# Performance work log

Measured on AMD Instinct MI355X. Metric: run time of the kernel, lower is better.

## Reference

```python
import jax, jax.numpy as jnp
import numpy as np

B, T, D, H = 2, 2048, 1024, 16
HD = D // H  # 64


def setup_inputs() -> dict:
    key = jax.random.key(0)
    ks = jax.random.split(key, 9)
    s = 1.0 / np.sqrt(D)
    return {
        "x": jax.random.normal(ks[0], (B, T, D), dtype=jnp.float32),
        "Wq": jax.random.uniform(ks[1], (D, D), minval=-s, maxval=s, dtype=jnp.float32),
        "bq": jax.random.uniform(ks[2], (D,), minval=-s, maxval=s, dtype=jnp.float32),
        "Wk": jax.random.uniform(ks[3], (D, D), minval=-s, maxval=s, dtype=jnp.float32),
        "bk": jax.random.uniform(ks[4], (D,), minval=-s, maxval=s, dtype=jnp.float32),
        "Wv": jax.random.uniform(ks[5], (D, D), minval=-s, maxval=s, dtype=jnp.float32),
        "bv": jax.random.uniform(ks[6], (D,), minval=-s, maxval=s, dtype=jnp.float32),
        "Wo": jax.random.uniform(ks[7], (D, D), minval=-s, maxval=s, dtype=jnp.float32),
        "bo": jax.random.uniform(ks[8], (D,), minval=-s, maxval=s, dtype=jnp.float32),
    }


def reference(x, Wq, bq, Wk, bk, Wv, bv, Wo, bo):
    b, t, d = x.shape
    # projections (nn.Linear: x @ W.T + b), split heads -> [B,H,T,hd]
    def split_heads(y):
        return y.reshape(b, t, H, HD).transpose(0, 2, 1, 3)
    Q = split_heads(x @ Wq.T + bq)
    K = split_heads(x @ Wk.T + bk)
    V = split_heads(x @ Wv.T + bv)
    # causal linear attention via cumulative outer-product state
    # Z[b,h,s,p,n] = V[b,h,s,p] * K[b,h,s,n]
    Z = jnp.einsum('bhsp,bhsn->bhspn', V, K)
    Z_cum = jnp.cumsum(Z, axis=2)  # prefix sum over time -> causal state
    Y = jnp.einsum('bhtn,bhtpn->bhtp', Q, Z_cum)  # [B,H,T,hd]
    Y = Y.transpose(0, 2, 1, 3).reshape(b, t, d)
    return Y @ Wo.T + bo
```

## Files before the change

kernel.cpp:

```cpp
#include <hip/hip_runtime.h>
#include <stdint.h>

#define B_  2
#define T_  2048
#define D_  1024
#define H_  16
#define HD_ 64
#define M_  (B_*T_)
#define CHK 128
#define NC  (T_/CHK)
#define BH  (B_*H_)

#define XN   4194304
#define WN   1048576

typedef unsigned short ushort_t;
typedef unsigned int   uint_t;

typedef __bf16 bf16x8 __attribute__((ext_vector_type(8)));
typedef float  f32x4  __attribute__((ext_vector_type(4)));

__device__ inline ushort_t f2bf(float f) {
    uint_t x = __float_as_uint(f);
    x += 0x7fffu + ((x >> 16) & 1u);
    return (ushort_t)(x >> 16);
}

__device__ inline uint4 pack8(const float4& lo, const float4& hi) {
    uint4 pk;
    pk.x = (uint_t)f2bf(lo.x) | ((uint_t)f2bf(lo.y) << 16);
    pk.y = (uint_t)f2bf(lo.z) | ((uint_t)f2bf(lo.w) << 16);
    pk.z = (uint_t)f2bf(hi.x) | ((uint_t)f2bf(hi.y) << 16);
    pk.w = (uint_t)f2bf(hi.z) | ((uint_t)f2bf(hi.w) << 16);
    return pk;
}

__global__ __launch_bounds__(256) void to_bf16_all(
    const float* __restrict__ x,  const float* __restrict__ Wq,
    const float* __restrict__ Wk, const float* __restrict__ Wv,
    const float* __restrict__ Wo, ushort_t* __restrict__ dst)
{
    const int idx = blockIdx.x * 256 + threadIdx.x;
    const int e   = idx * 8;
    const float* src;
    if      (e < XN)          src = x  + e;
    else if (e < XN + WN)     src = Wq + (e - XN);
    else if (e < XN + 2*WN)   src = Wk + (e - XN - WN);
    else if (e < XN + 3*WN)   src = Wv + (e - XN - 2*WN);
    else                      src = Wo + (e - XN - 3*WN);
    float4 lo = ((const float4*)src)[0];
    float4 hi = ((const float4*)src)[1];
    *(uint4*)(dst + e) = pack8(lo, hi);
}

__device__ inline void stage_rows(const ushort_t* __restrict__ g, ushort_t* ldsw,
                                  int lane, int issues) {
    const int rr  = lane >> 3;
    const int kg8 = ((lane & 7) ^ rr) << 3;
    const ushort_t* src = g + (size_t)rr * D_ + kg8;
    #pragma unroll
    for (int i = 0; i < issues; i++) {
        __builtin_amdgcn_global_load_lds(
            (const __attribute__((address_space(1))) void*)(src + (size_t)(i * 8) * D_),
            (__attribute__((address_space(3))) void*)(ldsw + i * 512),
            16, 0, 0);
    }
}

__global__ __launch_bounds__(256) void gemm_qkv(
    const ushort_t* __restrict__ xb, const ushort_t* __restrict__ Wqkvb,
    const float* __restrict__ bq, const float* __restrict__ bk,
    const float* __restrict__ bv, ushort_t* __restrict__ qkv_ws)
{
    const int flat = blockIdx.x;
    const int r    = flat & 7;
    const int j    = flat >> 3;
    const int mt   = ((r >> 1) << 4) | (j & 15);
    const int nt   = ((r & 1) << 2) | ((j >> 4) & 3);
    const int z    = j >> 6;

    const ushort_t* W  = Wqkvb + (size_t)z * WN;
    const float*    bi = (z == 0) ? bq : ((z == 1) ? bk : bv);
    ushort_t* out = qkv_ws + (size_t)z * (size_t)M_ * D_;

    __shared__ __align__(16) ushort_t As[64 * 64];
    __shared__ __align__(16) ushort_t Bs[128 * 64];

    const int tid  = threadIdx.x;
    const int m0   = mt * 64;
    const int n0   = nt * 128;
    const int wave = tid >> 6;
    const int lane = tid & 63;
    const int wm   = (wave >> 1) * 32;
    const int wn   = (wave & 1) * 64;
    const int fr   = lane & 15;
    const int quad = lane >> 4;

    const ushort_t* Ag = xb + (size_t)(m0 + wave * 16) * D_;
    const ushort_t* Bg = W  + (size_t)(n0 + wave * 32) * D_;
    ushort_t* Alds = &As[wave * 16 * 64];
    ushort_t* Blds = &Bs[wave * 32 * 64];

    f32x4 acc[2][4];
    #pragma unroll
    for (int i = 0; i < 2; i++)
        #pragma unroll
        for (int j2 = 0; j2 < 4; j2++)
            acc[i][j2] = (f32x4){0.f, 0.f, 0.f, 0.f};

    for (int k0 = 0; k0 < D_; k0 += 64) {
        __syncthreads();
        stage_rows(Ag + k0, Alds, lane, 2);
        stage_rows(Bg + k0, Blds, lane, 4);
        __syncthreads();

        #pragma unroll
        for (int ksg = 0; ksg <= 4; ksg += 4) {
            const int kgo = ((ksg + quad) ^ (fr & 7)) << 3;
            bf16x8 af[2], bf[4];
            #pragma unroll
            for (int i = 0; i < 2; i++) {
                uint4 u = *(const uint4*)&As[(wm + i * 16 + fr) * 64 + kgo];
                af[i] = __builtin_bit_cast(bf16x8, u);
            }
            #pragma unroll
            for (int j2 = 0; j2 < 4; j2++) {
                uint4 u = *(const uint4*)&Bs[(wn + j2 * 16 + fr) * 64 + kgo];
                bf[j2] = __builtin_bit_cast(bf16x8, u);
            }
            #pragma unroll
            for (int i = 0; i < 2; i++)
                #pragma unroll
                for (int j2 = 0; j2 < 4; j2++)
                    acc[i][j2] = __builtin_amdgcn_mfma_f32_16x16x32_bf16(
                        af[i], bf[j2], acc[i][j2], 0, 0, 0);
        }
    }

    const int rb = quad * 4;
    #pragma unroll
    for (int j2 = 0; j2 < 4; j2++) {
        const int n = n0 + wn + j2 * 16 + fr;
        const float bias = bi[n];
        const int h  = n >> 6;
        const int hd = n & 63;
        #pragma unroll
        for (int i = 0; i < 2; i++) {
            #pragma unroll
            for (int rr = 0; rr < 4; rr++) {
                const int m = m0 + wm + i * 16 + rb + rr;
                const int b = m >> 11, t = m & (T_ - 1);
                out[(((size_t)(b * H_ + h)) * T_ + t) * HD_ + hd] =
                    f2bf(acc[i][j2][rr] + bias);
            }
        }
    }
}

__global__ __launch_bounds__(256) void gemm_out(
    const ushort_t* __restrict__ Yw, const ushort_t* __restrict__ Wob,
    const float* __restrict__ bo, float* __restrict__ out)
{
    const int flat = blockIdx.x;
    const int r    = flat & 7;
    const int j    = flat >> 3;
    const int mt   = ((r >> 1) << 4) | (j & 15);
    const int nt   = ((r & 1) << 2) | (j >> 4);

    __shared__ __align__(16) ushort_t As[64 * 64];
    __shared__ __align__(16) ushort_t Bs[128 * 64];

    const int tid  = threadIdx.x;
    const int m0   = mt * 64;
    const int n0   = nt * 128;
    const int wave = tid >> 6;
    const int lane = tid & 63;
    const int wm   = (wave >> 1) * 32;
    const int wn   = (wave & 1) * 64;
    const int fr   = lane & 15;
    const int quad = lane >> 4;

    const ushort_t* Ag = Yw  + (size_t)(m0 + wave * 16) * D_;
    const ushort_t* Bg = Wob + (size_t)(n0 + wave * 32) * D_;
    ushort_t* Alds = &As[wave * 16 * 64];
    ushort_t* Blds = &Bs[wave * 32 * 64];

    f32x4 acc[2][4];
    #pragma unroll
    for (int i = 0; i < 2; i++)
        #pragma unroll
        for (int j2 = 0; j2 < 4; j2++)
            acc[i][j2] = (f32x4){0.f, 0.f, 0.f, 0.f};

    for (int k0 = 0; k0 < D_; k0 += 64) {
        __syncthreads();
        stage_rows(Ag + k0, Alds, lane, 2);
        stage_rows(Bg + k0, Blds, lane, 4);
        __syncthreads();

        #pragma unroll
        for (int ksg = 0; ksg <= 4; ksg += 4) {
            const int kgo = ((ksg + quad) ^ (fr & 7)) << 3;
            bf16x8 af[2], bf[4];
            #pragma unroll
            for (int i = 0; i < 2; i++) {
                uint4 u = *(const uint4*)&As[(wm + i * 16 + fr) * 64 + kgo];
                af[i] = __builtin_bit_cast(bf16x8, u);
            }
            #pragma unroll
            for (int j2 = 0; j2 < 4; j2++) {
                uint4 u = *(const uint4*)&Bs[(wn + j2 * 16 + fr) * 64 + kgo];
                bf[j2] = __builtin_bit_cast(bf16x8, u);
            }
            #pragma unroll
            for (int i = 0; i < 2; i++)
                #pragma unroll
                for (int j2 = 0; j2 < 4; j2++)
                    acc[i][j2] = __builtin_amdgcn_mfma_f32_16x16x32_bf16(
                        af[i], bf[j2], acc[i][j2], 0, 0, 0);
        }
    }

    const int rb = quad * 4;
    #pragma unroll
    for (int j2 = 0; j2 < 4; j2++) {
        const int n = n0 + wn + j2 * 16 + fr;
        const float bias = bo[n];
        #pragma unroll
        for (int i = 0; i < 2; i++) {
            #pragma unroll
            for (int rr = 0; rr < 4; rr++) {
                const int m = m0 + wm + i * 16 + rb + rr;
                out[(size_t)m * D_ + n] = acc[i][j2][rr] + bias;
            }
        }
    }
}

#define LDS_ 136

__device__ inline void scatter_T(const uint4* u, ushort_t* dst, int tid) {
    #pragma unroll
    for (int g = 0; g < 4; g++) {
        const int v  = tid + 256 * g;
        const int s  = v >> 3;
        const int p8 = (v & 7) * 8;
        ushort_t e[8];
        *(uint4*)e = u[g];
        const int sb = s >> 3, slo = s & 7;
        #pragma unroll
        for (int j = 0; j < 8; j++) {
            const int p   = p8 + j;
            const int blk = (sb & 8) | ((sb ^ (p >> 3)) & 7);
            dst[p * LDS_ + (blk << 3) + slo] = e[j];
        }
    }
}

__device__ inline void stage_T(const ushort_t* __restrict__ src, ushort_t* dst, int tid) {
    uint4 u[4];
    #pragma unroll
    for (int g = 0; g < 4; g++) u[g] = ((const uint4*)src)[tid + 256 * g];
    scatter_T(u, dst, tid);
}

__device__ inline void stage_T512(const ushort_t* __restrict__ src, ushort_t* dst, int tid) {
    uint4 u[2];
    #pragma unroll
    for (int g = 0; g < 2; g++) u[g] = ((const uint4*)src)[tid + 512 * g];
    #pragma unroll
    for (int g = 0; g < 2; g++) {
        const int v  = tid + 512 * g;
        const int s  = v >> 3;
        const int p8 = (v & 7) * 8;
        ushort_t e[8];
        *(uint4*)e = u[g];
        const int sb = s >> 3, slo = s & 7;
        #pragma unroll
        for (int j = 0; j < 8; j++) {
            const int p   = p8 + j;
            const int blk = (sb & 8) | ((sb ^ (p >> 3)) & 7);
            dst[p * LDS_ + (blk << 3) + slo] = e[j];
        }
    }
}

__global__ __launch_bounds__(256) void chunk_delta(
    const ushort_t* __restrict__ k_ws, const ushort_t* __restrict__ v_ws,
    float* __restrict__ delta)
{
    const int c  = blockIdx.x;
    const int bh = blockIdx.y;
    __shared__ __align__(16) ushort_t VtS[64 * LDS_];
    __shared__ __align__(16) ushort_t KtS[64 * LDS_];

    const int tid  = threadIdx.x;
    const int wave = tid >> 6, lane = tid & 63;
    const int fr = lane & 15, quad = lane >> 4, rb = quad * 4;
    const int p  = wave * 16 + fr;

    const size_t base = ((size_t)bh * T_ + (size_t)c * CHK) * HD_;
    stage_T(v_ws + base, VtS, tid);
    stage_T(k_ws + base, KtS, tid);
    __syncthreads();

    f32x4 acc[4];
    #pragma unroll
    for (int jn = 0; jn < 4; jn++) acc[jn] = (f32x4){0.f, 0.f, 0.f, 0.f};

    #pragma unroll
    for (int kt = 0; kt < 4; kt++) {
        const int sb   = kt * 4 + quad;
        const int blkA = (sb & 8) | ((sb ^ (p >> 3)) & 7);
        bf16x8 af = __builtin_bit_cast(bf16x8,
            *(const uint4*)&VtS[p * LDS_ + (blkA << 3)]);
        #pragma unroll
        for (int jn = 0; jn < 4; jn++) {
            const int nr   = jn * 16 + fr;
            const int blkB = (sb & 8) | ((sb ^ (nr >> 3)) & 7);
            uint4 ub = *(const uint4*)&KtS[nr * LDS_ + (blkB << 3)];
            acc[jn] = __builtin_amdgcn_mfma_f32_16x16x32_bf16(
                af, __builtin_bit_cast(bf16x8, ub), acc[jn], 0, 0, 0);
        }
    }

    float* dp = delta + ((size_t)bh * NC + c) * 4096;
    #pragma unroll
    for (int jn = 0; jn < 4; jn++)
        #pragma unroll
        for (int r = 0; r < 4; r++)
            dp[(wave * 16 + rb + r) * 64 + jn * 16 + fr] = acc[jn][r];
}

__global__ __launch_bounds__(256) void states_prefix(
    const float* __restrict__ delta, ushort_t* __restrict__ states_bf)
{
    const int qd = blockIdx.x;
    const int bh = blockIdx.y;
    const size_t b0 = (size_t)bh * NC * 4096 + qd * 1024 + threadIdx.x;

    float s[4] = {0.f, 0.f, 0.f, 0.f};
    #pragma unroll
    for (int c = 0; c < NC; c++) {
        #pragma unroll
        for (int u = 0; u < 4; u++) {
            const size_t o = b0 + (size_t)c * 4096 + u * 256;
            states_bf[o] = f2bf(s[u]);
            s[u] += delta[o];
        }
    }
}

__global__ __launch_bounds__(512) void attn_chunk(
    const ushort_t* __restrict__ q_ws, const ushort_t* __restrict__ k_ws,
    const ushort_t* __restrict__ v_ws, const ushort_t* __restrict__ states_bf,
    ushort_t* __restrict__ y_ws)
{
    const int c = blockIdx.x, bh = blockIdx.y;
    __shared__ __align__(16) ushort_t VtS[64 * LDS_];
    __shared__ __align__(16) ushort_t Smat[128 * LDS_];

    const int tid  = threadIdx.x;
    const int wave = tid >> 6;
    const int lane = tid & 63;
    const int fr   = lane & 15;
    const int quad = lane >> 4;
    const int fk   = quad * 8;
    const int rb   = quad * 4;

    const size_t base = ((size_t)bh * T_ + (size_t)c * CHK) * HD_;
    const ushort_t* qg = q_ws + base;
    const ushort_t* kg = k_ws + base;
    const ushort_t* vg = v_ws + base;
    const ushort_t* st = states_bf + ((size_t)bh * NC + c) * 4096;

    stage_T512(vg, VtS, tid);
    __syncthreads();

    const int m = wave;

    bf16x8 aq[2];
    #pragma unroll
    for (int kk = 0; kk < 2; kk++) {
        uint4 u = *(const uint4*)(qg + (m * 16 + fr) * HD_ + kk * 32 + fk);
        aq[kk] = __builtin_bit_cast(bf16x8, u);
    }

    f32x4 acc[4];
    #pragma unroll
    for (int jn = 0; jn < 4; jn++) acc[jn] = (f32x4){0.f, 0.f, 0.f, 0.f};

    #pragma unroll
    for (int jn = 0; jn < 4; jn++) {
        #pragma unroll
        for (int kk = 0; kk < 2; kk++) {
            uint4 u = *(const uint4*)(st + (jn * 16 + fr) * 64 + kk * 32 + fk);
            bf16x8 bsp = __builtin_bit_cast(bf16x8, u);
            acc[jn] = __builtin_amdgcn_mfma_f32_16x16x32_bf16(
                aq[kk], bsp, acc[jn], 0, 0, 0);
        }
    }

    const int nk = (m + 2) >> 1;
    const int jt = 2 * nk;

    f32x4 sc[8];
    #pragma unroll
    for (int j = 0; j < 8; j++) sc[j] = (f32x4){0.f, 0.f, 0.f, 0.f};

    #pragma unroll
    for (int j = 0; j < 8; j++) {
        if (j <= m) {
            #pragma unroll
            for (int kk = 0; kk < 2; kk++) {
                uint4 u = *(const uint4*)(kg + (j * 16 + fr) * HD_ + kk * 32 + fk);
                sc[j] = __builtin_amdgcn_mfma_f32_16x16x32_bf16(
                    aq[kk], __builtin_bit_cast(bf16x8, u), sc[j], 0, 0, 0);
            }
        }
    }

    #pragma unroll
    for (int j = 0; j < 8; j++) {
        if (j < jt) {
            f32x4 v = sc[j];
            if (j == m) {
                #pragma unroll
                for (int r = 0; r < 4; r++)
                    if (fr > rb + r) v[r] = 0.f;
            }
            #pragma unroll
            for (int r = 0; r < 4; r++)
                Smat[(m * 16 + rb + r) * LDS_ + j * 16 + fr] = f2bf(v[r]);
        }
    }

    #pragma unroll
    for (int kt = 0; kt < 4; kt++) {
        if (kt < nk) {
            uint4 ua = *(const uint4*)&Smat[(m * 16 + fr) * LDS_ + kt * 32 + fk];
            bf16x8 as_ = __builtin_bit_cast(bf16x8, ua);
            #pragma unroll
            for (int jn = 0; jn < 4; jn++) {
                const int p   = jn * 16 + fr;
                const int sb  = kt * 4 + quad;
                const int blk = (sb & 8) | ((sb ^ (p >> 3)) & 7);
                uint4 ub = *(const uint4*)&VtS[p * LDS_ + (blk << 3)];
                acc[jn] = __builtin_amdgcn_mfma_f32_16x16x32_bf16(
                    as_, __builtin_bit_cast(bf16x8, ub), acc[jn], 0, 0, 0);
            }
        }
    }

    const int b = bh >> 4, h = bh & 15;
    ushort_t* yg = y_ws + ((size_t)(b * T_ + c * CHK)) * D_ + h * 64;
    #pragma unroll
    for (int jn = 0; jn < 4; jn++) {
        #pragma unroll
        for (int r = 0; r < 4; r++) {
            const int t = m * 16 + rb + r;
            const int p = jn * 16 + fr;
            yg[(size_t)t * D_ + p] = f2bf(acc[jn][r]);
        }
    }
}

extern "C" void kernel_launch(void* const* d_in, const int* in_sizes, int n_in,
                              void* d_out, int out_size, void* d_ws, size_t ws_size,
                              hipStream_t stream)
{
    const float* x  = (const float*)d_in[0];
    const float* Wq = (const float*)d_in[1];
    const float* bq = (const float*)d_in[2];
    const float* Wk = (const float*)d_in[3];
    const float* bk = (const float*)d_in[4];
    const float* Wv = (const float*)d_in[5];
    const float* bv = (const float*)d_in[6];
    const float* Wo = (const float*)d_in[7];
    const float* bo = (const float*)d_in[8];
    float* out = (float*)d_out;

    ushort_t* cvt    = (ushort_t*)d_ws;
    ushort_t* xb     = cvt;
    ushort_t* Wqkvb  = cvt + (size_t)XN;
    ushort_t* Wob    = cvt + (size_t)XN + 3 * WN;
    ushort_t* q_ws   = cvt + (size_t)XN + 4 * WN;
    ushort_t* k_ws   = q_ws + (size_t)M_ * D_;
    ushort_t* v_ws   = k_ws + (size_t)M_ * D_;
    ushort_t* y_ws   = v_ws + (size_t)M_ * D_;
    ushort_t* states_bf = Wqkvb;
    float*    delta  = (float*)(y_ws + (size_t)M_ * D_);

    to_bf16_all<<<dim3((XN + 4 * WN) / 8 / 256), 256, 0, stream>>>(
        x, Wq, Wk, Wv, Wo, cvt);
    gemm_qkv<<<dim3(1536), 256, 0, stream>>>(
        xb, Wqkvb, bq, bk, bv, q_ws);
    chunk_delta<<<dim3(NC, BH), 256, 0, stream>>>(k_ws, v_ws, delta);
    states_prefix<<<dim3(4, BH), 256, 0, stream>>>(delta, states_bf);
    attn_chunk<<<dim3(NC, BH), 512, 0, stream>>>(q_ws, k_ws, v_ws, states_bf, y_ws);
    gemm_out<<<dim3(512), 256, 0, stream>>>(y_ws, Wob, bo, out);
}
```

Baseline: 162.4 us.

## Fuse chunk-state prefix sum into attention kernel, drop states_prefix launch

Removes the separate states_prefix kernel, which ran a sequential scan over chunks using only 128 blocks. Each attn_chunk block now sums the fp32 deltas of all preceding chunks itself, converts the result to bf16 in shared memory, and feeds it to the MFMA inter-chunk term. Chunk 0 skips this term. This saves a launch and the low-parallelism scan, at the cost of redundant O(c) delta reads per block, up to 15 chunks of 16KB each.

```diff
diff --git a/kernel.cpp b/kernel.cpp
--- a/kernel.cpp
+++ b/kernel.cpp
@@ -332,33 +332,16 @@
             dp[(wave * 16 + rb + r) * 64 + jn * 16 + fr] = acc[jn][r];
 }
 
-__global__ __launch_bounds__(256) void states_prefix(
-    const float* __restrict__ delta, ushort_t* __restrict__ states_bf)
-{
-    const int qd = blockIdx.x;
-    const int bh = blockIdx.y;
-    const size_t b0 = (size_t)bh * NC * 4096 + qd * 1024 + threadIdx.x;
-
-    float s[4] = {0.f, 0.f, 0.f, 0.f};
-    #pragma unroll
-    for (int c = 0; c < NC; c++) {
-        #pragma unroll
-        for (int u = 0; u < 4; u++) {
-            const size_t o = b0 + (size_t)c * 4096 + u * 256;
-            states_bf[o] = f2bf(s[u]);
-            s[u] += delta[o];
-        }
-    }
-}
-
+#define STS_ 72
 __global__ __launch_bounds__(512) void attn_chunk(
     const ushort_t* __restrict__ q_ws, const ushort_t* __restrict__ k_ws,
-    const ushort_t* __restrict__ v_ws, const ushort_t* __restrict__ states_bf,
+    const ushort_t* __restrict__ v_ws, const float* __restrict__ delta,
     ushort_t* __restrict__ y_ws)
 {
     const int c = blockIdx.x, bh = blockIdx.y;
     __shared__ __align__(16) ushort_t VtS[64 * LDS_];
     __shared__ __align__(16) ushort_t Smat[128 * LDS_];
+    __shared__ __align__(16) ushort_t StS[64 * STS_];
 
     const int tid  = threadIdx.x;
     const int wave = tid >> 6;
@@ -372,9 +355,26 @@
     const ushort_t* qg = q_ws + base;
     const ushort_t* kg = k_ws + base;
     const ushort_t* vg = v_ws + base;
-    const ushort_t* st = states_bf + ((size_t)bh * NC + c) * 4096;
 
     stage_T512(vg, VtS, tid);
+
+    if (c > 0) {
+        float s[8];
+        #pragma unroll
+        for (int i = 0; i < 8; i++) s[i] = 0.f;
+        const float* dbase = delta + (size_t)bh * NC * 4096 + tid * 8;
+        for (int cc = 0; cc < c; cc++) {
+            const float* dp = dbase + (size_t)cc * 4096;
+            float4 a = ((const float4*)dp)[0];
+            float4 b = ((const float4*)dp)[1];
+            s[0] += a.x; s[1] += a.y; s[2] += a.z; s[3] += a.w;
+            s[4] += b.x; s[5] += b.y; s[6] += b.z; s[7] += b.w;
+        }
+        ushort_t ev[8];
+        #pragma unroll
+        for (int i = 0; i < 8; i++) ev[i] = f2bf(s[i]);
+        *(uint4*)&StS[(tid >> 3) * STS_ + (tid & 7) * 8] = *(uint4*)ev;
+    }
     __syncthreads();
 
     const int m = wave;
@@ -390,14 +390,16 @@
     #pragma unroll
     for (int jn = 0; jn < 4; jn++) acc[jn] = (f32x4){0.f, 0.f, 0.f, 0.f};
 
-    #pragma unroll
-    for (int jn = 0; jn < 4; jn++) {
-        #pragma unroll
-        for (int kk = 0; kk < 2; kk++) {
-            uint4 u = *(const uint4*)(st + (jn * 16 + fr) * 64 + kk * 32 + fk);
-            bf16x8 bsp = __builtin_bit_cast(bf16x8, u);
-            acc[jn] = __builtin_amdgcn_mfma_f32_16x16x32_bf16(
-                aq[kk], bsp, acc[jn], 0, 0, 0);
+    if (c > 0) {
+        #pragma unroll
+        for (int jn = 0; jn < 4; jn++) {
+            #pragma unroll
+            for (int kk = 0; kk < 2; kk++) {
+                uint4 u = *(const uint4*)&StS[(jn * 16 + fr) * STS_ + kk * 32 + fk];
+                bf16x8 bsp = __builtin_bit_cast(bf16x8, u);
+                acc[jn] = __builtin_amdgcn_mfma_f32_16x16x32_bf16(
+                    aq[kk], bsp, acc[jn], 0, 0, 0);
+            }
         }
     }
 
@@ -488,7 +490,6 @@
     ushort_t* k_ws   = q_ws + (size_t)M_ * D_;
     ushort_t* v_ws   = k_ws + (size_t)M_ * D_;
     ushort_t* y_ws   = v_ws + (size_t)M_ * D_;
-    ushort_t* states_bf = Wqkvb;
     float*    delta  = (float*)(y_ws + (size_t)M_ * D_);
 
     to_bf16_all<<<dim3((XN + 4 * WN) / 8 / 256), 256, 0, stream>>>(
@@ -496,7 +497,6 @@
     gemm_qkv<<<dim3(1536), 256, 0, stream>>>(
         xb, Wqkvb, bq, bk, bv, q_ws);
     chunk_delta<<<dim3(NC, BH), 256, 0, stream>>>(k_ws, v_ws, delta);
-    states_prefix<<<dim3(4, BH), 256, 0, stream>>>(delta, states_bf);
-    attn_chunk<<<dim3(NC, BH), 512, 0, stream>>>(q_ws, k_ws, v_ws, states_bf, y_ws);
+    attn_chunk<<<dim3(NC, BH), 512, 0, stream>>>(q_ws, k_ws, v_ws, delta, y_ws);
     gemm_out<<<dim3(512), 256, 0, stream>>>(y_ws, Wob, bo, out);
 }
```

Result: slower. 167.4 us (+3.1%).

## Fuse Q/K/V projections into one block sharing the staged x tile

Applied to the files above, without the earlier changes.

The QKV GEMM now has each 512-thread block compute a 128x64 tile for all three projections at once. The x tile is staged into LDS once and reused against three weight tiles, so x is read from memory a third as often. The grid shrinks from 1536 to 512 blocks. Each wave now holds 12 accumulators instead of 8, which raises register pressure, and the smaller grid may balance less evenly across CUs.

```diff
diff --git a/kernel.cpp b/kernel.cpp
--- a/kernel.cpp
+++ b/kernel.cpp
@@ -67,91 +67,100 @@
     }
 }
 
-__global__ __launch_bounds__(256) void gemm_qkv(
+__global__ __launch_bounds__(512) void gemm_qkv(
     const ushort_t* __restrict__ xb, const ushort_t* __restrict__ Wqkvb,
     const float* __restrict__ bq, const float* __restrict__ bk,
     const float* __restrict__ bv, ushort_t* __restrict__ qkv_ws)
 {
-    const int flat = blockIdx.x;
-    const int r    = flat & 7;
-    const int j    = flat >> 3;
-    const int mt   = ((r >> 1) << 4) | (j & 15);
-    const int nt   = ((r & 1) << 2) | ((j >> 4) & 3);
-    const int z    = j >> 6;
-
-    const ushort_t* W  = Wqkvb + (size_t)z * WN;
-    const float*    bi = (z == 0) ? bq : ((z == 1) ? bk : bv);
-    ushort_t* out = qkv_ws + (size_t)z * (size_t)M_ * D_;
-
-    __shared__ __align__(16) ushort_t As[64 * 64];
-    __shared__ __align__(16) ushort_t Bs[128 * 64];
+    const int bid = blockIdx.x;
+    const int r   = bid & 7;
+    const int j   = bid >> 3;
+    const int mt  = ((r >> 1) << 3) | (j & 7);
+    const int nt  = ((r & 1) << 3) | (j >> 3);
+    const int m0  = mt * 128;
+    const int n0  = nt * 64;
+
+    __shared__ __align__(16) ushort_t As[128 * 64];
+    __shared__ __align__(16) ushort_t Bs[3 * 64 * 64];
 
     const int tid  = threadIdx.x;
-    const int m0   = mt * 64;
-    const int n0   = nt * 128;
     const int wave = tid >> 6;
     const int lane = tid & 63;
     const int wm   = (wave >> 1) * 32;
-    const int wn   = (wave & 1) * 64;
+    const int wn   = (wave & 1) * 32;
     const int fr   = lane & 15;
     const int quad = lane >> 4;
+    const int rb   = quad * 4;
 
     const ushort_t* Ag = xb + (size_t)(m0 + wave * 16) * D_;
-    const ushort_t* Bg = W  + (size_t)(n0 + wave * 32) * D_;
     ushort_t* Alds = &As[wave * 16 * 64];
-    ushort_t* Blds = &Bs[wave * 32 * 64];
-
-    f32x4 acc[2][4];
-    #pragma unroll
-    for (int i = 0; i < 2; i++)
-        #pragma unroll
-        for (int j2 = 0; j2 < 4; j2++)
-            acc[i][j2] = (f32x4){0.f, 0.f, 0.f, 0.f};
+
+    f32x4 acc[3][2][2];
+    #pragma unroll
+    for (int z = 0; z < 3; z++)
+        #pragma unroll
+        for (int i = 0; i < 2; i++)
+            #pragma unroll
+            for (int j2 = 0; j2 < 2; j2++)
+                acc[z][i][j2] = (f32x4){0.f, 0.f, 0.f, 0.f};
 
     for (int k0 = 0; k0 < D_; k0 += 64) {
         __syncthreads();
         stage_rows(Ag + k0, Alds, lane, 2);
-        stage_rows(Bg + k0, Blds, lane, 4);
+        #pragma unroll
+        for (int z = 0; z < 3; z++) {
+            const ushort_t* Bg = Wqkvb + (size_t)z * WN
+                               + (size_t)(n0 + wave * 8) * D_;
+            stage_rows(Bg + k0, &Bs[z * 4096 + wave * 8 * 64], lane, 1);
+        }
         __syncthreads();
 
         #pragma unroll
         for (int ksg = 0; ksg <= 4; ksg += 4) {
             const int kgo = ((ksg + quad) ^ (fr & 7)) << 3;
-            bf16x8 af[2], bf[4];
+            bf16x8 af[2];
             #pragma unroll
             for (int i = 0; i < 2; i++) {
                 uint4 u = *(const uint4*)&As[(wm + i * 16 + fr) * 64 + kgo];
                 af[i] = __builtin_bit_cast(bf16x8, u);
             }
             #pragma unroll
-            for (int j2 = 0; j2 < 4; j2++) {
-                uint4 u = *(const uint4*)&Bs[(wn + j2 * 16 + fr) * 64 + kgo];
-                bf[j2] = __builtin_bit_cast(bf16x8, u);
-            }
-            #pragma unroll
-            for (int i = 0; i < 2; i++)
+            for (int z = 0; z < 3; z++) {
+                bf16x8 bf[2];
                 #pragma unroll
-                for (int j2 = 0; j2 < 4; j2++)
-                    acc[i][j2] = __builtin_amdgcn_mfma_f32_16x16x32_bf16(
-                        af[i], bf[j2], acc[i][j2], 0, 0, 0);
-        }
-    }
-
-    const int rb = quad * 4;
-    #pragma unroll
-    for (int j2 = 0; j2 < 4; j2++) {
-        const int n = n0 + wn + j2 * 16 + fr;
-        const float bias = bi[n];
-        const int h  = n >> 6;
-        const int hd = n & 63;
-        #pragma unroll
-        for (int i = 0; i < 2; i++) {
-            #pragma unroll
-            for (int rr = 0; rr < 4; rr++) {
-                const int m = m0 + wm + i * 16 + rb + rr;
-                const int b = m >> 11, t = m & (T_ - 1);
-                out[(((size_t)(b * H_ + h)) * T_ + t) * HD_ + hd] =
-                    f2bf(acc[i][j2][rr] + bias);
+                for (int j2 = 0; j2 < 2; j2++) {
+                    uint4 u = *(const uint4*)&Bs[z * 4096 + (wn + j2 * 16 + fr) * 64 + kgo];
+                    bf[j2] = __builtin_bit_cast(bf16x8, u);
+                }
+                #pragma unroll
+                for (int i = 0; i < 2; i++)
+                    #pragma unroll
+                    for (int j2 = 0; j2 < 2; j2++)
+                        acc[z][i][j2] = __builtin_amdgcn_mfma_f32_16x16x32_bf16(
+                            af[i], bf[j2], acc[z][i][j2], 0, 0, 0);
+            }
+        }
+    }
+
+    #pragma unroll
+    for (int z = 0; z < 3; z++) {
+        const float* bi = (z == 0) ? bq : ((z == 1) ? bk : bv);
+        ushort_t*    oz = qkv_ws + (size_t)z * (size_t)M_ * D_;
+        #pragma unroll
+        for (int j2 = 0; j2 < 2; j2++) {
+            const int n = n0 + wn + j2 * 16 + fr;
+            const float bias = bi[n];
+            const int h  = n >> 6;
+            const int hd = n & 63;
+            #pragma unroll
+            for (int i = 0; i < 2; i++) {
+                #pragma unroll
+                for (int rr = 0; rr < 4; rr++) {
+                    const int m = m0 + wm + i * 16 + rb + rr;
+                    const int b = m >> 11, t = m & (T_ - 1);
+                    oz[(((size_t)(b * H_ + h)) * T_ + t) * HD_ + hd] =
+                        f2bf(acc[z][i][j2][rr] + bias);
+                }
             }
         }
     }
@@ -493,7 +502,7 @@
 
     to_bf16_all<<<dim3((XN + 4 * WN) / 8 / 256), 256, 0, stream>>>(
         x, Wq, Wk, Wv, Wo, cvt);
-    gemm_qkv<<<dim3(1536), 256, 0, stream>>>(
+    gemm_qkv<<<dim3(512), 512, 0, stream>>>(
         xb, Wqkvb, bq, bk, bv, q_ws);
     chunk_delta<<<dim3(NC, BH), 256, 0, stream>>>(k_ws, v_ws, delta);
     states_prefix<<<dim3(4, BH), 256, 0, stream>>>(delta, states_bf);
```

Result: no change. 161.9 us (-0.3%).
